# Optimization experiments

Hardware: AMD Instinct MI355X
Metric: run time of the kernel (lower is better)

## Reference

```python
import jax, jax.numpy as jnp
import numpy as np

B, CIN, H, W = 16, 256, 56, 56
D, HEADS, KS, PAD, STRIDE, M = 256, 8, 3, 1, 1, 4
K = KS * KS
N = D // HEADS
# relative_indices: sum of window coords, flattened row-major, values in [0, 2*KS-2]
REL = (np.arange(KS)[:, None] + np.arange(KS)[None, :]).reshape(-1)


def setup_inputs() -> dict:
    key = jax.random.key(0)
    ks = jax.random.split(key, 7)
    return {
        "x": jax.random.normal(ks[0], (B, CIN, H, W), jnp.float32),
        "q": jax.random.normal(ks[1], (B, D, 1), jnp.float32),
        "Wk": jax.random.normal(ks[2], (D, CIN), jnp.float32) * 0.05,
        "Wv": jax.random.normal(ks[3], (D, CIN), jnp.float32) * 0.05,
        "pos_emb": jax.random.normal(ks[4], (1, 2 * KS - 1), jnp.float32),
        "Wlin": jax.random.normal(ks[5], (1, M), jnp.float32),
        "Wproj": jax.random.normal(ks[6], (D, D), jnp.float32) * 0.05,
    }


def _unfold(t):
    # torch nn.Unfold: (B,C,H,W) -> (B, C*K, L); patches feature dim ordered (C, kh, kw)
    p = jax.lax.conv_general_dilated_patches(
        t, (KS, KS), (STRIDE, STRIDE), [(PAD, PAD), (PAD, PAD)])
    b, _, ho, wo = p.shape
    return p.reshape(b, -1, ho * wo), ho, wo


def reference(x, q, Wk, Wv, pos_emb, Wlin, Wproj):
    b = x.shape[0]
    k = jnp.einsum('oc,bchw->bohw', Wk, x)  # 1x1 conv, no bias
    v = jnp.einsum('oc,bchw->bohw', Wv, x)
    ku, ho, wo = _unfold(k)
    vu, _, _ = _unfold(v)
    L = ho * wo
    ku = ku.reshape(b, HEADS, N, K, L)  # (b, h, n, k, l)
    vu = vu.reshape(b, HEADS, N, K, L)
    qh = q.reshape(b, HEADS, N)  # learned per-batch query, d=1 squeezed
    attn = jnp.einsum('bhn,bhnkl->bhlk', qh, ku)  # (b,h,l,K)
    attn = attn + pos_emb[0, REL]  # relative position bias, shape (K,)
    attn = jax.nn.softmax(attn, axis=-1)
    # repeat d(=1) -> m identical rows then Linear(m,1,no bias): equals scale by sum(Wlin)
    attn = attn * jnp.sum(Wlin)
    out = jnp.einsum('bhlk,bhnkl->bhnl', attn, vu)  # (b,h,n,l)
    out = out.reshape(b, D, ho, wo)  # fold with kernel 1 == reshape
    return jnp.einsum('oc,bchw->bohw', Wproj, out)  # 1x1 proj conv
```

## Files before the change

kernel.cpp:

```cpp
#include <hip/hip_runtime.h>

#define B_     16
#define D_     256
#define HEADS_ 8
#define N_     32
#define H_     56
#define W_     56
#define L_     3136
#define BL_    (B_ * L_)
#define LDA_A  264

typedef short short8 __attribute__((ext_vector_type(8)));
typedef float f32x4  __attribute__((ext_vector_type(4)));

__device__ __forceinline__ unsigned short f2bf(float f) {
    union { float f; unsigned u; } c; c.f = f;
    unsigned u = c.u;
    u += 0x7fffu + ((u >> 16) & 1u);
    return (unsigned short)(u >> 16);
}

__global__ __launch_bounds__(256) void convert_w_kernel(
    const float* __restrict__ Wv, const float* __restrict__ Wproj,
    const float* __restrict__ Wk, const float* __restrict__ q,
    unsigned short* __restrict__ Wvb, unsigned short* __restrict__ Wpb,
    float* __restrict__ qt)
{
    if (blockIdx.y < 2) {
        const float* src   = (blockIdx.y == 0) ? Wv  : Wproj;
        unsigned short* dst = (blockIdx.y == 0) ? Wvb : Wpb;
        const int i = (blockIdx.x * 256 + threadIdx.x) * 4;
        float4 v = *(const float4*)(src + i);
        uint2 o;
        o.x = (unsigned)f2bf(v.x) | ((unsigned)f2bf(v.y) << 16);
        o.y = (unsigned)f2bf(v.z) | ((unsigned)f2bf(v.w) << 16);
        *(uint2*)(dst + i) = o;
    } else {
        const int b  = blockIdx.x >> 2;
        const int h0 = (blockIdx.x & 3) * 2;
        const int c  = threadIdx.x;
#pragma unroll
        for (int hh = 0; hh < 2; ++hh) {
            const int h = h0 + hh;
            const float* qb = q  + b * D_ + h * N_;
            const float* wr = Wk + (size_t)(h * N_) * D_ + c;
            float acc = 0.f;
#pragma unroll 8
            for (int n = 0; n < N_; ++n)
                acc = fmaf(qb[n], wr[(size_t)n * D_], acc);
            qt[((size_t)b * HEADS_ + h) * D_ + c] = acc;
        }
    }
}

__global__ __launch_bounds__(256) void s_kernel(
    const float* __restrict__ x, const float* __restrict__ qt,
    float* __restrict__ S)
{
    __shared__ float  qs[HEADS_ * D_];
    __shared__ float4 red[8][HEADS_][32];

    const int bb = blockIdx.y;
    const int l0 = blockIdx.x * 128;
    const int t  = threadIdx.x;
    const int lg = t & 31;
    const int cg = t >> 5;

    {
        const float4* s4 = (const float4*)(qt + (size_t)bb * HEADS_ * D_);
        ((float4*)qs)[t]       = s4[t];
        ((float4*)qs)[t + 256] = s4[t + 256];
    }
    __syncthreads();

    float4 sacc[8];
#pragma unroll
    for (int h = 0; h < 8; ++h) sacc[h] = (float4){0.f, 0.f, 0.f, 0.f};

    const int l = l0 + lg * 4;
    if (l < L_) {
        const float* xb = x + (size_t)bb * D_ * L_ + l;
#pragma unroll 4
        for (int c = cg * 32; c < cg * 32 + 32; ++c) {
            const float4 xv = *(const float4*)(xb + (size_t)c * L_);
#pragma unroll
            for (int h = 0; h < 8; ++h) {
                const float qv = qs[h * D_ + c];
                sacc[h].x = fmaf(qv, xv.x, sacc[h].x);
                sacc[h].y = fmaf(qv, xv.y, sacc[h].y);
                sacc[h].z = fmaf(qv, xv.z, sacc[h].z);
                sacc[h].w = fmaf(qv, xv.w, sacc[h].w);
            }
        }
    }

#pragma unroll
    for (int h = 0; h < 8; ++h) red[cg][h][lg] = sacc[h];
    __syncthreads();

    {
        const int h  = t >> 5;
        const int l2 = t & 31;
        const int lw = l0 + l2 * 4;
        if (lw < L_) {
            float4 o = (float4){0.f, 0.f, 0.f, 0.f};
#pragma unroll
            for (int g = 0; g < 8; ++g) {
                const float4 v = red[g][h][l2];
                o.x += v.x; o.y += v.y; o.z += v.z; o.w += v.w;
            }
            *(float4*)(S + ((size_t)bb * HEADS_ + h) * L_ + lw) = o;
        }
    }
}

__global__ __launch_bounds__(256) void gemm_v_mfma(
    const float* __restrict__ x, const unsigned short* __restrict__ Wvb,
    unsigned short* __restrict__ Vo)
{
    __shared__ __align__(16) unsigned short As[128 * LDA_A];

    const int t = threadIdx.x;
    const int w = t >> 6, lane = t & 63, col = lane & 15, quad = lane >> 4;
    const int wr = w >> 1, wc = w & 1;
    const int n0 = blockIdx.x * 128;
    const int d0 = blockIdx.y * 128;

#pragma unroll
    for (int i = 0; i < 16; ++i) {
        const int u   = t + i * 256;
        const int row = u >> 5;
        const int cu  = (u & 31) * 8;
        uint4 v = *(const uint4*)(Wvb + (size_t)(d0 + row) * D_ + cu);
        *(uint4*)&As[row * LDA_A + cu] = v;
    }

    const float* xb[4];
#pragma unroll
    for (int n = 0; n < 4; ++n) {
        const unsigned flat = n0 + wc * 64 + n * 16 + col;
        const unsigned bq = flat / L_;
        const unsigned lq = flat - bq * L_;
        xb[n] = x + ((size_t)bq * D_ + quad * 8) * L_ + lq;
    }

    f32x4 acc[4][4];
#pragma unroll
    for (int m = 0; m < 4; ++m)
#pragma unroll
        for (int n = 0; n < 4; ++n) acc[m][n] = (f32x4){0.f, 0.f, 0.f, 0.f};

    __syncthreads();

#pragma unroll
    for (int kt = 0; kt < 8; ++kt) {
        short8 bf[4];
#pragma unroll
        for (int n = 0; n < 4; ++n) {
            float f[8];
#pragma unroll
            for (int j = 0; j < 8; ++j)
                f[j] = xb[n][(size_t)(kt * 32 + j) * L_];
            union { unsigned u[4]; short8 s; } pk;
#pragma unroll
            for (int p = 0; p < 4; ++p)
                asm("v_cvt_pk_bf16_f32 %0, %1, %2"
                    : "=v"(pk.u[p]) : "v"(f[2 * p]), "v"(f[2 * p + 1]));
            bf[n] = pk.s;
        }
        short8 af[4];
#pragma unroll
        for (int m = 0; m < 4; ++m)
            af[m] = *(const short8*)&As[(wr * 64 + m * 16 + col) * LDA_A + kt * 32 + quad * 8];
#pragma unroll
        for (int m = 0; m < 4; ++m)
#pragma unroll
            for (int n = 0; n < 4; ++n)
                acc[m][n] = __builtin_amdgcn_mfma_f32_16x16x32_bf16(af[m], bf[n], acc[m][n], 0, 0, 0);
    }

#pragma unroll
    for (int n = 0; n < 4; ++n) {
        const unsigned flat = n0 + wc * 64 + n * 16 + col;
        const unsigned bq = flat / L_;
        const unsigned lq = flat - bq * L_;
#pragma unroll
        for (int m = 0; m < 4; ++m) {
            const int d  = d0 + wr * 64 + m * 16 + quad * 4;
            const int h  = d >> 5;
            const int dn = d & 31;
            unsigned short ob[4];
#pragma unroll
            for (int r = 0; r < 4; ++r) ob[r] = f2bf(acc[m][n][r]);
            *(uint2*)(Vo + ((size_t)(bq * HEADS_ + h) * L_ + lq) * N_ + dn) =
                *(const uint2*)ob;
        }
    }
}

__global__ __launch_bounds__(256) void attend_kernel(
    const float* __restrict__ S, const unsigned short* __restrict__ Vo,
    const float* __restrict__ pos_emb, const float* __restrict__ Wlin,
    unsigned short* __restrict__ Om)
{
    __shared__ __align__(16) unsigned short Vs[600 * 32];
    __shared__ float Ss[10][58];

    const int band = blockIdx.x;
    const int bh   = blockIdx.y;
    const int y0   = band * 8;
    const int t    = threadIdx.x;

    const float* Sb = S + (size_t)bh * L_;
    for (int wi = t; wi < 580; wi += 256) {
        const int row = wi / 58, c = wi - row * 58;
        const int gr = y0 - 1 + row, gc = c - 1;
        float v = 0.f;
        if (gr >= 0 && gr < H_ && gc >= 0 && gc < W_)
            v = Sb[gr * W_ + gc];
        Ss[row][c] = v;
    }

    const unsigned short* Vbase = Vo + (size_t)bh * L_ * N_;
    for (int wi = t; wi < 2400; wi += 256) {
        const int p = wi >> 2, i = wi & 3;
        const int row = p / 60, cc = p - row * 60;
        const int gr = y0 - 1 + row, gc = cc - 1;
        uint4 v = make_uint4(0u, 0u, 0u, 0u);
        if (gr >= 0 && gr < H_ && gc >= 0 && gc < W_)
            v = *(const uint4*)(Vbase + (size_t)(gr * W_ + gc) * N_ + i * 8);
        const int sfc = wi ^ (p & 7);
        *(uint4*)(Vs + sfc * 8) = v;
    }
    __syncthreads();

    const float scale = Wlin[0] + Wlin[1] + Wlin[2] + Wlin[3];
    const float pe0 = pos_emb[0], pe1 = pos_emb[1], pe2 = pos_emb[2];
    const float pe3 = pos_emb[3], pe4 = pos_emb[4];
    const float bias[9] = {pe0, pe1, pe2, pe1, pe2, pe3, pe2, pe3, pe4};

    for (int idx = t; idx < 448; idx += 256) {
        const int yl = idx / 56, xx = idx - yl * 56;
        const int lr = yl + 1, lc = xx + 1;

        float lg[9], m = -1e30f;
#pragma unroll
        for (int dy = 0; dy < 3; ++dy)
#pragma unroll
            for (int dx = 0; dx < 3; ++dx) {
                const int k = dy * 3 + dx;
                lg[k] = Ss[lr - 1 + dy][lc - 1 + dx] + bias[k];
                m = fmaxf(m, lg[k]);
            }
        float ssum = 0.f;
#pragma unroll
        for (int k = 0; k < 9; ++k) { lg[k] = __expf(lg[k] - m); ssum += lg[k]; }
        const float inv = scale / ssum;

        float om[32];
#pragma unroll
        for (int i = 0; i < 32; ++i) om[i] = 0.f;

#pragma unroll
        for (int dy = 0; dy < 3; ++dy)
#pragma unroll
            for (int dx = 0; dx < 3; ++dx) {
                const float wk = lg[dy * 3 + dx] * inv;
                const int pos  = (lr - 1 + dy) * 60 + (lc - 1 + dx);
                const int base = pos * 4;
                const int msk  = pos & 7;
#pragma unroll
                for (int i = 0; i < 4; ++i) {
                    const int sfc = (base + i) ^ msk;
                    const uint4 v = *(const uint4*)(Vs + sfc * 8);
                    const unsigned* u = (const unsigned*)&v;
#pragma unroll
                    for (int j = 0; j < 4; ++j) {
                        union { unsigned uu; float f; } lo, hi;
                        lo.uu = u[j] << 16;
                        hi.uu = u[j] & 0xffff0000u;
                        om[i * 8 + 2 * j]     = fmaf(wk, lo.f, om[i * 8 + 2 * j]);
                        om[i * 8 + 2 * j + 1] = fmaf(wk, hi.f, om[i * 8 + 2 * j + 1]);
                    }
                }
            }

        unsigned short ob[32];
#pragma unroll
        for (int i = 0; i < 32; ++i) ob[i] = f2bf(om[i]);
        const int l = (y0 + yl) * W_ + xx;
        uint4* dst = (uint4*)(Om + ((size_t)bh * L_ + l) * N_);
        const uint4* sb = (const uint4*)ob;
#pragma unroll
        for (int i = 0; i < 4; ++i) dst[i] = sb[i];
    }
}

__global__ __launch_bounds__(256) void gemm_proj_mfma(
    const unsigned short* __restrict__ Om, const unsigned short* __restrict__ Wpb,
    float* __restrict__ Out)
{
    __shared__ __align__(16) unsigned short As[128 * LDA_A];

    const int t = threadIdx.x;
    const int w = t >> 6, lane = t & 63, col = lane & 15, quad = lane >> 4;
    const int wr = w >> 1, wc = w & 1;
    const int n0 = blockIdx.x * 128;
    const int d0 = blockIdx.y * 128;

#pragma unroll
    for (int i = 0; i < 16; ++i) {
        const int u   = t + i * 256;
        const int row = u >> 5;
        const int cu  = (u & 31) * 8;
        uint4 v = *(const uint4*)(Wpb + (size_t)(d0 + row) * D_ + cu);
        *(uint4*)&As[row * LDA_A + cu] = v;
    }

    const unsigned short* ob[4];
#pragma unroll
    for (int n = 0; n < 4; ++n) {
        const unsigned flat = n0 + wc * 64 + n * 16 + col;
        const unsigned bq = flat / L_;
        const unsigned lq = flat - bq * L_;
        ob[n] = Om + ((size_t)(bq * HEADS_) * L_ + lq) * N_ + quad * 8;
    }
    const size_t kstride = (size_t)L_ * N_;

    f32x4 acc[4][4];
#pragma unroll
    for (int m = 0; m < 4; ++m)
#pragma unroll
        for (int n = 0; n < 4; ++n) acc[m][n] = (f32x4){0.f, 0.f, 0.f, 0.f};

    __syncthreads();

#pragma unroll
    for (int kt = 0; kt < 8; ++kt) {
        short8 bf[4], af[4];
#pragma unroll
        for (int n = 0; n < 4; ++n)
            bf[n] = *(const short8*)(ob[n] + (size_t)kt * kstride);
#pragma unroll
        for (int m = 0; m < 4; ++m)
            af[m] = *(const short8*)&As[(wr * 64 + m * 16 + col) * LDA_A + kt * 32 + quad * 8];
#pragma unroll
        for (int m = 0; m < 4; ++m)
#pragma unroll
            for (int n = 0; n < 4; ++n)
                acc[m][n] = __builtin_amdgcn_mfma_f32_16x16x32_bf16(af[m], bf[n], acc[m][n], 0, 0, 0);
    }

#pragma unroll
    for (int n = 0; n < 4; ++n) {
        const unsigned flat = n0 + wc * 64 + n * 16 + col;
        const unsigned bq = flat / L_;
        const unsigned lq = flat - bq * L_;
        float* oout = Out + (size_t)bq * D_ * L_ + lq;
#pragma unroll
        for (int m = 0; m < 4; ++m) {
            const int dbase = d0 + wr * 64 + m * 16 + quad * 4;
#pragma unroll
            for (int r = 0; r < 4; ++r)
                oout[(size_t)(dbase + r) * L_] = acc[m][n][r];
        }
    }
}

extern "C" void kernel_launch(void* const* d_in, const int* in_sizes, int n_in,
                              void* d_out, int out_size, void* d_ws, size_t ws_size,
                              hipStream_t stream)
{
    const float* x       = (const float*)d_in[0];
    const float* q       = (const float*)d_in[1];
    const float* Wk      = (const float*)d_in[2];
    const float* Wv      = (const float*)d_in[3];
    const float* pos_emb = (const float*)d_in[4];
    const float* Wlin    = (const float*)d_in[5];
    const float* Wproj   = (const float*)d_in[6];
    float* out = (float*)d_out;

    const size_t planeE = (size_t)B_ * D_ * L_;
    unsigned short* Vo  = (unsigned short*)d_ws;
    unsigned short* Om  = Vo + planeE;
    unsigned short* Wvb = Om + planeE;
    unsigned short* Wpb = Wvb + D_ * D_;
    float*          S   = (float*)(Wpb + D_ * D_);
    float*          qt  = S + (size_t)B_ * HEADS_ * L_;

    convert_w_kernel<<<dim3(64, 3), 256, 0, stream>>>(Wv, Wproj, Wk, q, Wvb, Wpb, qt);
    s_kernel<<<dim3((L_ + 127) / 128, B_), 256, 0, stream>>>(x, qt, S);
    gemm_v_mfma<<<dim3(BL_ / 128, 2), 256, 0, stream>>>(x, Wvb, Vo);
    attend_kernel<<<dim3(7, B_ * HEADS_), 256, 0, stream>>>(S, Vo, pos_emb, Wlin, Om);
    gemm_proj_mfma<<<dim3(BL_ / 128, 2), 256, 0, stream>>>(Om, Wpb, out);
}
```

Before: 174.6 us.

## Double-buffer V-projection GEMM tiles via LDS with async global-to-LDS weight loads

Restructures the V projection GEMM to stream both operands through double-buffered shared memory per 32-wide k-slice instead of preloading all weights and reading x straight from global with strided scalar loads. Weights are copied with global_load_lds into an XOR-swizzled tile, and x is loaded as float4 along L, transposed into a padded LDS tile, then converted to bf16 on read. The goal is coalesced x loads and overlap of the next slice's loads with the current MFMAs. The cost is two extra barriers per k-step and more LDS traffic.

Measured after the change: 179.3 us. 2.7% more time.

```diff
diff --git a/kernel.cpp b/kernel.cpp
--- a/kernel.cpp
+++ b/kernel.cpp
@@ -9,6 +9,7 @@
 #define L_     3136
 #define BL_    (B_ * L_)
 #define LDA_A  264
+#define LDB_V  36
 
 typedef short short8 __attribute__((ext_vector_type(8)));
 typedef float f32x4  __attribute__((ext_vector_type(4)));
@@ -19,6 +20,10 @@
     u += 0x7fffu + ((u >> 16) & 1u);
     return (unsigned short)(u >> 16);
 }
+
+#define GL2L(g, l) __builtin_amdgcn_global_load_lds( \
+    (const __attribute__((address_space(1))) void*)(g), \
+    (__attribute__((address_space(3))) void*)(l), 16, 0, 0)
 
 __global__ __launch_bounds__(256) void convert_w_kernel(
     const float* __restrict__ Wv, const float* __restrict__ Wproj,
@@ -118,7 +123,8 @@
     const float* __restrict__ x, const unsigned short* __restrict__ Wvb,
     unsigned short* __restrict__ Vo)
 {
-    __shared__ __align__(16) unsigned short As[128 * LDA_A];
+    __shared__ unsigned short As[2][128 * 32];
+    __shared__ __align__(16) float Bs[2][128 * LDB_V];
 
     const int t = threadIdx.x;
     const int w = t >> 6, lane = t & 63, col = lane & 15, quad = lane >> 4;
@@ -126,22 +132,19 @@
     const int n0 = blockIdx.x * 128;
     const int d0 = blockIdx.y * 128;
 
-#pragma unroll
-    for (int i = 0; i < 16; ++i) {
-        const int u   = t + i * 256;
-        const int row = u >> 5;
-        const int cu  = (u & 31) * 8;
-        uint4 v = *(const uint4*)(Wvb + (size_t)(d0 + row) * D_ + cu);
-        *(uint4*)&As[row * LDA_A + cu] = v;
-    }
-
-    const float* xb[4];
-#pragma unroll
-    for (int n = 0; n < 4; ++n) {
-        const unsigned flat = n0 + wc * 64 + n * 16 + col;
-        const unsigned bq = flat / L_;
-        const unsigned lq = flat - bq * L_;
-        xb[n] = x + ((size_t)bq * D_ + quad * 8) * L_ + lq;
+    const int srow = t >> 2;
+    const int skc  = (((t & 3) ^ ((t >> 3) & 3))) * 8;
+    const unsigned short* Ag = Wvb + (size_t)(d0 + srow) * D_ + skc;
+
+    const int cB = t & 31;
+    const float* bp[4];
+#pragma unroll
+    for (int i = 0; i < 4; ++i) {
+        const int lt   = ((t >> 5) + i * 8) * 4;
+        const int flat = n0 + lt;
+        const unsigned bq = (unsigned)flat / L_;
+        const unsigned lq = (unsigned)flat - bq * L_;
+        bp[i] = x + (size_t)bq * D_ * L_ + (size_t)cB * L_ + lq;
     }
 
     f32x4 acc[4][4];
@@ -150,33 +153,73 @@
 #pragma unroll
         for (int n = 0; n < 4; ++n) acc[m][n] = (f32x4){0.f, 0.f, 0.f, 0.f};
 
-    __syncthreads();
+    float4 pv[4];
+    {
+        char* An = (char*)&As[0][0] + w * 1024;
+        GL2L(Ag, An);            GL2L(Ag + 64 * D_, An + 4096);
+#pragma unroll
+        for (int i = 0; i < 4; ++i) pv[i] = *(const float4*)bp[i];
+        __syncthreads();
+#pragma unroll
+        for (int i = 0; i < 4; ++i) {
+            const int lti = ((t >> 5) + i * 8) * 4;
+#pragma unroll
+            for (int j = 0; j < 4; ++j)
+                Bs[0][(lti + j) * LDB_V + cB] = ((const float*)&pv[i])[j];
+        }
+        __syncthreads();
+    }
 
 #pragma unroll
     for (int kt = 0; kt < 8; ++kt) {
+        const int cur = kt & 1;
+        if (kt < 7) {
+            const int c1 = (kt + 1) * 32;
+            char* An = (char*)&As[cur ^ 1][0] + w * 1024;
+            GL2L(Ag + c1, An);       GL2L(Ag + 64 * D_ + c1, An + 4096);
+#pragma unroll
+            for (int i = 0; i < 4; ++i)
+                pv[i] = *(const float4*)(bp[i] + (size_t)c1 * L_);
+        }
+
+        short8 af[4];
+#pragma unroll
+        for (int m = 0; m < 4; ++m) {
+            const int row = wr * 64 + m * 16 + col;
+            const int chk = quad ^ ((row >> 1) & 3);
+            af[m] = *(const short8*)(&As[cur][0] + row * 32 + chk * 8);
+        }
         short8 bf[4];
 #pragma unroll
         for (int n = 0; n < 4; ++n) {
-            float f[8];
-#pragma unroll
-            for (int j = 0; j < 8; ++j)
-                f[j] = xb[n][(size_t)(kt * 32 + j) * L_];
+            const int l = wc * 64 + n * 16 + col;
+            const float* br = &Bs[cur][l * LDB_V + quad * 8];
+            const float4 v0 = *(const float4*)br;
+            const float4 v1 = *(const float4*)(br + 4);
             union { unsigned u[4]; short8 s; } pk;
-#pragma unroll
-            for (int p = 0; p < 4; ++p)
-                asm("v_cvt_pk_bf16_f32 %0, %1, %2"
-                    : "=v"(pk.u[p]) : "v"(f[2 * p]), "v"(f[2 * p + 1]));
+            asm("v_cvt_pk_bf16_f32 %0, %1, %2" : "=v"(pk.u[0]) : "v"(v0.x), "v"(v0.y));
+            asm("v_cvt_pk_bf16_f32 %0, %1, %2" : "=v"(pk.u[1]) : "v"(v0.z), "v"(v0.w));
+            asm("v_cvt_pk_bf16_f32 %0, %1, %2" : "=v"(pk.u[2]) : "v"(v1.x), "v"(v1.y));
+            asm("v_cvt_pk_bf16_f32 %0, %1, %2" : "=v"(pk.u[3]) : "v"(v1.z), "v"(v1.w));
             bf[n] = pk.s;
         }
-        short8 af[4];
-#pragma unroll
-        for (int m = 0; m < 4; ++m)
-            af[m] = *(const short8*)&As[(wr * 64 + m * 16 + col) * LDA_A + kt * 32 + quad * 8];
 #pragma unroll
         for (int m = 0; m < 4; ++m)
 #pragma unroll
             for (int n = 0; n < 4; ++n)
                 acc[m][n] = __builtin_amdgcn_mfma_f32_16x16x32_bf16(af[m], bf[n], acc[m][n], 0, 0, 0);
+
+        __syncthreads();
+        if (kt < 7) {
+#pragma unroll
+            for (int i = 0; i < 4; ++i) {
+                const int lti = ((t >> 5) + i * 8) * 4;
+#pragma unroll
+                for (int j = 0; j < 4; ++j)
+                    Bs[cur ^ 1][(lti + j) * LDB_V + cB] = ((const float*)&pv[i])[j];
+            }
+        }
+        __syncthreads();
     }
 
 #pragma unroll
```

## Fuse score computation into V GEMM via extra MFMA, retile GEMMs to 64x64

Applied to the files above, without the earlier changes.

Removes the separate s_kernel. The per-head scores are now computed in gemm_v_mfma as an extra 16-row MFMA against a bf16, zero-padded q·Wk matrix, reusing the x fragments already loaded for the V projection. Both GEMMs move to 64x64 tiles on a (L/64, 4, B) grid, which avoids per-column batch division, and they register-double-buffer the B-operand loads. The projection GEMM stages its output through LDS so it can write coalesced float4 rows. Scores are now computed in bf16 instead of fp32, which reduces accuracy, and every y-block recomputes the S MFMAs even though only the y==0 blocks store them.

After: 185.5 us. +6.3%, slower.

```diff
diff --git a/kernel.cpp b/kernel.cpp
--- a/kernel.cpp
+++ b/kernel.cpp
@@ -7,7 +7,6 @@
 #define H_     56
 #define W_     56
 #define L_     3136
-#define BL_    (B_ * L_)
 #define LDA_A  264
 
 typedef short short8 __attribute__((ext_vector_type(8)));
@@ -24,7 +23,7 @@
     const float* __restrict__ Wv, const float* __restrict__ Wproj,
     const float* __restrict__ Wk, const float* __restrict__ q,
     unsigned short* __restrict__ Wvb, unsigned short* __restrict__ Wpb,
-    float* __restrict__ qt)
+    unsigned short* __restrict__ qtb)
 {
     if (blockIdx.y < 2) {
         const float* src   = (blockIdx.y == 0) ? Wv  : Wproj;
@@ -48,152 +47,124 @@
 #pragma unroll 8
             for (int n = 0; n < N_; ++n)
                 acc = fmaf(qb[n], wr[(size_t)n * D_], acc);
-            qt[((size_t)b * HEADS_ + h) * D_ + c] = acc;
-        }
-    }
-}
-
-__global__ __launch_bounds__(256) void s_kernel(
-    const float* __restrict__ x, const float* __restrict__ qt,
-    float* __restrict__ S)
-{
-    __shared__ float  qs[HEADS_ * D_];
-    __shared__ float4 red[8][HEADS_][32];
-
-    const int bb = blockIdx.y;
-    const int l0 = blockIdx.x * 128;
-    const int t  = threadIdx.x;
-    const int lg = t & 31;
-    const int cg = t >> 5;
-
-    {
-        const float4* s4 = (const float4*)(qt + (size_t)bb * HEADS_ * D_);
-        ((float4*)qs)[t]       = s4[t];
-        ((float4*)qs)[t + 256] = s4[t + 256];
-    }
-    __syncthreads();
-
-    float4 sacc[8];
-#pragma unroll
-    for (int h = 0; h < 8; ++h) sacc[h] = (float4){0.f, 0.f, 0.f, 0.f};
-
-    const int l = l0 + lg * 4;
-    if (l < L_) {
-        const float* xb = x + (size_t)bb * D_ * L_ + l;
-#pragma unroll 4
-        for (int c = cg * 32; c < cg * 32 + 32; ++c) {
-            const float4 xv = *(const float4*)(xb + (size_t)c * L_);
-#pragma unroll
-            for (int h = 0; h < 8; ++h) {
-                const float qv = qs[h * D_ + c];
-                sacc[h].x = fmaf(qv, xv.x, sacc[h].x);
-                sacc[h].y = fmaf(qv, xv.y, sacc[h].y);
-                sacc[h].z = fmaf(qv, xv.z, sacc[h].z);
-                sacc[h].w = fmaf(qv, xv.w, sacc[h].w);
-            }
-        }
-    }
-
-#pragma unroll
-    for (int h = 0; h < 8; ++h) red[cg][h][lg] = sacc[h];
-    __syncthreads();
-
-    {
-        const int h  = t >> 5;
-        const int l2 = t & 31;
-        const int lw = l0 + l2 * 4;
-        if (lw < L_) {
-            float4 o = (float4){0.f, 0.f, 0.f, 0.f};
-#pragma unroll
-            for (int g = 0; g < 8; ++g) {
-                const float4 v = red[g][h][l2];
-                o.x += v.x; o.y += v.y; o.z += v.z; o.w += v.w;
-            }
-            *(float4*)(S + ((size_t)bb * HEADS_ + h) * L_ + lw) = o;
+            qtb[((size_t)b * 16 + h) * D_ + c]     = f2bf(acc);
+            qtb[((size_t)b * 16 + 8 + h) * D_ + c] = 0;
         }
     }
 }
 
 __global__ __launch_bounds__(256) void gemm_v_mfma(
     const float* __restrict__ x, const unsigned short* __restrict__ Wvb,
-    unsigned short* __restrict__ Vo)
-{
-    __shared__ __align__(16) unsigned short As[128 * LDA_A];
+    const unsigned short* __restrict__ qtb,
+    unsigned short* __restrict__ Vo, float* __restrict__ S)
+{
+    __shared__ __align__(16) unsigned short As[64 * LDA_A];
 
     const int t = threadIdx.x;
     const int w = t >> 6, lane = t & 63, col = lane & 15, quad = lane >> 4;
     const int wr = w >> 1, wc = w & 1;
-    const int n0 = blockIdx.x * 128;
-    const int d0 = blockIdx.y * 128;
-
-#pragma unroll
-    for (int i = 0; i < 16; ++i) {
-        const int u   = t + i * 256;
-        const int row = u >> 5;
-        const int cu  = (u & 31) * 8;
-        uint4 v = *(const uint4*)(Wvb + (size_t)(d0 + row) * D_ + cu);
-        *(uint4*)&As[row * LDA_A + cu] = v;
-    }
-
-    const float* xb[4];
-#pragma unroll
-    for (int n = 0; n < 4; ++n) {
-        const unsigned flat = n0 + wc * 64 + n * 16 + col;
-        const unsigned bq = flat / L_;
-        const unsigned lq = flat - bq * L_;
-        xb[n] = x + ((size_t)bq * D_ + quad * 8) * L_ + lq;
-    }
-
-    f32x4 acc[4][4];
-#pragma unroll
-    for (int m = 0; m < 4; ++m)
-#pragma unroll
-        for (int n = 0; n < 4; ++n) acc[m][n] = (f32x4){0.f, 0.f, 0.f, 0.f};
+    const int bb = blockIdx.z;
+    const int d0 = blockIdx.y * 64;
+    const int l0 = blockIdx.x * 64;
+    const bool doS = (blockIdx.y == 0);
+
+#pragma unroll
+    for (int i = 0; i < 8; ++i) {
+        const int u = t + i * 256;
+        const int row = u >> 5, cu = (u & 31) * 8;
+        *(uint4*)&As[row * LDA_A + cu] =
+            *(const uint4*)(Wvb + (size_t)(d0 + row) * D_ + cu);
+    }
+
+    const float* xg[2];
+#pragma unroll
+    for (int n = 0; n < 2; ++n)
+        xg[n] = x + (size_t)bb * D_ * L_ + (size_t)(quad * 8) * L_
+                  + l0 + wc * 32 + n * 16 + col;
+    const unsigned short* qg = qtb + ((size_t)bb * 16 + col) * D_ + quad * 8;
+
+    f32x4 acc[2][2], accS[2];
+#pragma unroll
+    for (int m = 0; m < 2; ++m)
+#pragma unroll
+        for (int n = 0; n < 2; ++n) acc[m][n] = (f32x4){0.f, 0.f, 0.f, 0.f};
+#pragma unroll
+    for (int n = 0; n < 2; ++n) accS[n] = (f32x4){0.f, 0.f, 0.f, 0.f};
+
+    float pB[2][2][8];
+    uint4 pQ[2];
+#pragma unroll
+    for (int n = 0; n < 2; ++n)
+#pragma unroll
+        for (int j = 0; j < 8; ++j)
+            pB[0][n][j] = xg[n][(size_t)j * L_];
+    pQ[0] = *(const uint4*)qg;
 
     __syncthreads();
 
 #pragma unroll
     for (int kt = 0; kt < 8; ++kt) {
-        short8 bf[4];
-#pragma unroll
-        for (int n = 0; n < 4; ++n) {
-            float f[8];
-#pragma unroll
-            for (int j = 0; j < 8; ++j)
-                f[j] = xb[n][(size_t)(kt * 32 + j) * L_];
+        const int cur = kt & 1, nxt = cur ^ 1;
+        if (kt < 7) {
+#pragma unroll
+            for (int n = 0; n < 2; ++n)
+#pragma unroll
+                for (int j = 0; j < 8; ++j)
+                    pB[nxt][n][j] = xg[n][(size_t)((kt + 1) * 32 + j) * L_];
+            pQ[nxt] = *(const uint4*)(qg + (kt + 1) * 32);
+        }
+
+        short8 bf[2];
+#pragma unroll
+        for (int n = 0; n < 2; ++n) {
             union { unsigned u[4]; short8 s; } pk;
 #pragma unroll
             for (int p = 0; p < 4; ++p)
-                asm("v_cvt_pk_bf16_f32 %0, %1, %2"
-                    : "=v"(pk.u[p]) : "v"(f[2 * p]), "v"(f[2 * p + 1]));
+                asm("v_cvt_pk_bf16_f32 %0, %1, %2" : "=v"(pk.u[p])
+                    : "v"(pB[cur][n][2 * p]), "v"(pB[cur][n][2 * p + 1]));
             bf[n] = pk.s;
         }
-        short8 af[4];
-#pragma unroll
-        for (int m = 0; m < 4; ++m)
-            af[m] = *(const short8*)&As[(wr * 64 + m * 16 + col) * LDA_A + kt * 32 + quad * 8];
-#pragma unroll
-        for (int m = 0; m < 4; ++m)
-#pragma unroll
-            for (int n = 0; n < 4; ++n)
-                acc[m][n] = __builtin_amdgcn_mfma_f32_16x16x32_bf16(af[m], bf[n], acc[m][n], 0, 0, 0);
-    }
-
-#pragma unroll
-    for (int n = 0; n < 4; ++n) {
-        const unsigned flat = n0 + wc * 64 + n * 16 + col;
-        const unsigned bq = flat / L_;
-        const unsigned lq = flat - bq * L_;
-#pragma unroll
-        for (int m = 0; m < 4; ++m) {
-            const int d  = d0 + wr * 64 + m * 16 + quad * 4;
-            const int h  = d >> 5;
-            const int dn = d & 31;
+        short8 af[2];
+#pragma unroll
+        for (int m = 0; m < 2; ++m)
+            af[m] = *(const short8*)&As[(wr * 32 + m * 16 + col) * LDA_A
+                                        + kt * 32 + quad * 8];
+        const short8 aq = *(const short8*)&pQ[cur];
+
+#pragma unroll
+        for (int m = 0; m < 2; ++m)
+#pragma unroll
+            for (int n = 0; n < 2; ++n)
+                acc[m][n] = __builtin_amdgcn_mfma_f32_16x16x32_bf16(
+                    af[m], bf[n], acc[m][n], 0, 0, 0);
+#pragma unroll
+        for (int n = 0; n < 2; ++n)
+            accS[n] = __builtin_amdgcn_mfma_f32_16x16x32_bf16(
+                aq, bf[n], accS[n], 0, 0, 0);
+    }
+
+#pragma unroll
+    for (int n = 0; n < 2; ++n) {
+        const int l = l0 + wc * 32 + n * 16 + col;
+#pragma unroll
+        for (int m = 0; m < 2; ++m) {
+            const int h  = (d0 >> 5) + wr;
+            const int dn = m * 16 + quad * 4;
             unsigned short ob[4];
 #pragma unroll
             for (int r = 0; r < 4; ++r) ob[r] = f2bf(acc[m][n][r]);
-            *(uint2*)(Vo + ((size_t)(bq * HEADS_ + h) * L_ + lq) * N_ + dn) =
+            *(uint2*)(Vo + ((size_t)(bb * HEADS_ + h) * L_ + l) * N_ + dn) =
                 *(const uint2*)ob;
+        }
+    }
+
+    if (doS && quad < 2) {
+#pragma unroll
+        for (int n = 0; n < 2; ++n) {
+            const int l = l0 + wc * 32 + n * 16 + col;
+#pragma unroll
+            for (int r = 0; r < 4; ++r)
+                S[((size_t)bb * HEADS_ + quad * 4 + r) * L_ + l] = accS[n][r];
         }
     }
 }
@@ -300,70 +271,83 @@
     const unsigned short* __restrict__ Om, const unsigned short* __restrict__ Wpb,
     float* __restrict__ Out)
 {
-    __shared__ __align__(16) unsigned short As[128 * LDA_A];
+    __shared__ __align__(16) char smem[64 * LDA_A * 2];
+    unsigned short* As = (unsigned short*)smem;
+    float*          Cs = (float*)smem;
 
     const int t = threadIdx.x;
     const int w = t >> 6, lane = t & 63, col = lane & 15, quad = lane >> 4;
     const int wr = w >> 1, wc = w & 1;
-    const int n0 = blockIdx.x * 128;
-    const int d0 = blockIdx.y * 128;
-
-#pragma unroll
-    for (int i = 0; i < 16; ++i) {
-        const int u   = t + i * 256;
-        const int row = u >> 5;
-        const int cu  = (u & 31) * 8;
-        uint4 v = *(const uint4*)(Wpb + (size_t)(d0 + row) * D_ + cu);
-        *(uint4*)&As[row * LDA_A + cu] = v;
-    }
-
-    const unsigned short* ob[4];
-#pragma unroll
-    for (int n = 0; n < 4; ++n) {
-        const unsigned flat = n0 + wc * 64 + n * 16 + col;
-        const unsigned bq = flat / L_;
-        const unsigned lq = flat - bq * L_;
-        ob[n] = Om + ((size_t)(bq * HEADS_) * L_ + lq) * N_ + quad * 8;
+    const int bb = blockIdx.z;
+    const int d0 = blockIdx.y * 64;
+    const int l0 = blockIdx.x * 64;
+
+#pragma unroll
+    for (int i = 0; i < 8; ++i) {
+        const int u = t + i * 256;
+        const int row = u >> 5, cu = (u & 31) * 8;
+        *(uint4*)&As[row * LDA_A + cu] =
+            *(const uint4*)(Wpb + (size_t)(d0 + row) * D_ + cu);
+    }
+
+    const unsigned short* og[2];
+#pragma unroll
+    for (int n = 0; n < 2; ++n) {
+        const int l = l0 + wc * 32 + n * 16 + col;
+        og[n] = Om + ((size_t)(bb * HEADS_) * L_ + l) * N_ + quad * 8;
     }
     const size_t kstride = (size_t)L_ * N_;
 
-    f32x4 acc[4][4];
-#pragma unroll
-    for (int m = 0; m < 4; ++m)
-#pragma unroll
-        for (int n = 0; n < 4; ++n) acc[m][n] = (f32x4){0.f, 0.f, 0.f, 0.f};
+    f32x4 acc[2][2];
+#pragma unroll
+    for (int m = 0; m < 2; ++m)
+#pragma unroll
+        for (int n = 0; n < 2; ++n) acc[m][n] = (f32x4){0.f, 0.f, 0.f, 0.f};
+
+    uint4 pB[2][2];
+#pragma unroll
+    for (int n = 0; n < 2; ++n) pB[0][n] = *(const uint4*)og[n];
 
     __syncthreads();
 
 #pragma unroll
     for (int kt = 0; kt < 8; ++kt) {
-        short8 bf[4], af[4];
-#pragma unroll
-        for (int n = 0; n < 4; ++n)
-            bf[n] = *(const short8*)(ob[n] + (size_t)kt * kstride);
-#pragma unroll
-        for (int m = 0; m < 4; ++m)
-            af[m] = *(const short8*)&As[(wr * 64 + m * 16 + col) * LDA_A + kt * 32 + quad * 8];
-#pragma unroll
-        for (int m = 0; m < 4; ++m)
-#pragma unroll
-            for (int n = 0; n < 4; ++n)
-                acc[m][n] = __builtin_amdgcn_mfma_f32_16x16x32_bf16(af[m], bf[n], acc[m][n], 0, 0, 0);
-    }
-
-#pragma unroll
-    for (int n = 0; n < 4; ++n) {
-        const unsigned flat = n0 + wc * 64 + n * 16 + col;
-        const unsigned bq = flat / L_;
-        const unsigned lq = flat - bq * L_;
-        float* oout = Out + (size_t)bq * D_ * L_ + lq;
-#pragma unroll
-        for (int m = 0; m < 4; ++m) {
-            const int dbase = d0 + wr * 64 + m * 16 + quad * 4;
+        const int cur = kt & 1, nxt = cur ^ 1;
+        if (kt < 7) {
+#pragma unroll
+            for (int n = 0; n < 2; ++n)
+                pB[nxt][n] = *(const uint4*)(og[n] + (size_t)(kt + 1) * kstride);
+        }
+        short8 af[2];
+#pragma unroll
+        for (int m = 0; m < 2; ++m)
+            af[m] = *(const short8*)&As[(wr * 32 + m * 16 + col) * LDA_A
+                                        + kt * 32 + quad * 8];
+#pragma unroll
+        for (int m = 0; m < 2; ++m)
+#pragma unroll
+            for (int n = 0; n < 2; ++n)
+                acc[m][n] = __builtin_amdgcn_mfma_f32_16x16x32_bf16(
+                    af[m], *(const short8*)&pB[cur][n], acc[m][n], 0, 0, 0);
+    }
+
+    __syncthreads();
+#pragma unroll
+    for (int m = 0; m < 2; ++m)
+#pragma unroll
+        for (int n = 0; n < 2; ++n)
 #pragma unroll
             for (int r = 0; r < 4; ++r)
-                oout[(size_t)(dbase + r) * L_] = acc[m][n][r];
-        }
+                Cs[(wr * 32 + m * 16 + quad * 4 + r) * 68
+                   + wc * 32 + n * 16 + col] = acc[m][n][r];
+    __syncthreads();
+
+    float* ob = Out + (size_t)bb * D_ * L_ + (size_t)d0 * L_ + l0;
+#pragma unroll
+    for (int i = 0; i < 4; ++i) {
+        const int u = t + i * 256;
+        const int row = u >> 4, lc = (u & 15) * 4;
+        *(float4*)(ob + (size_t)row * L_ + lc) = *(const float4*)&Cs[row * 68 + lc];
     }
 }
 
@@ -386,11 +370,10 @@
     unsigned short* Wvb = Om + planeE;
     unsigned short* Wpb = Wvb + D_ * D_;
     float*          S   = (float*)(Wpb + D_ * D_);
-    float*          qt  = S + (size_t)B_ * HEADS_ * L_;
-
-    convert_w_kernel<<<dim3(64, 3), 256, 0, stream>>>(Wv, Wproj, Wk, q, Wvb, Wpb, qt);
-    s_kernel<<<dim3((L_ + 127) / 128, B_), 256, 0, stream>>>(x, qt, S);
-    gemm_v_mfma<<<dim3(BL_ / 128, 2), 256, 0, stream>>>(x, Wvb, Vo);
+    unsigned short* qtb = (unsigned short*)(S + (size_t)B_ * HEADS_ * L_);
+
+    convert_w_kernel<<<dim3(64, 3), 256, 0, stream>>>(Wv, Wproj, Wk, q, Wvb, Wpb, qtb);
+    gemm_v_mfma<<<dim3(L_ / 64, 4, B_), 256, 0, stream>>>(x, Wvb, qtb, Vo, S);
     attend_kernel<<<dim3(7, B_ * HEADS_), 256, 0, stream>>>(S, Vo, pos_emb, Wlin, Om);
-    gemm_proj_mfma<<<dim3(BL_ / 128, 2), 256, 0, stream>>>(Om, Wpb, out);
-}
+    gemm_proj_mfma<<<dim3(L_ / 64, 4, B_), 256, 0, stream>>>(Om, Wpb, out);
+}
```
